# Performance work log

Measured on AMD Instinct MI355X. Metric: run time of the kernel, lower is better.

## Reference

```python
import jax, jax.numpy as jnp
import numpy as np

N_EMBD = 768
N_HEAD = 12
HEAD_DIM = N_EMBD // N_HEAD


def setup_inputs() -> dict:
    key = jax.random.key(0)
    k0, k1, k2, k3, k4 = jax.random.split(key, 5)
    B, T, C = 2, 4096, N_EMBD
    x = jax.random.normal(k0, (B, T, C), dtype=jnp.float32)
    # c_attn: Linear(C, 3C); c_proj: Linear(C, C). torch Linear: y = x @ W.T + b
    s = 1.0 / np.sqrt(C)
    W_attn = jax.random.uniform(k1, (3 * C, C), dtype=jnp.float32, minval=-s, maxval=s)
    b_attn = jax.random.uniform(k2, (3 * C,), dtype=jnp.float32, minval=-s, maxval=s)
    W_proj = jax.random.uniform(k3, (C, C), dtype=jnp.float32, minval=-s, maxval=s)
    b_proj = jax.random.uniform(k4, (C,), dtype=jnp.float32, minval=-s, maxval=s)
    return {"x": x, "W_attn": W_attn, "b_attn": b_attn, "W_proj": W_proj, "b_proj": b_proj}


def reference(x, W_attn, b_attn, W_proj, b_proj):
    B, T, C = x.shape
    H, D = N_HEAD, HEAD_DIM
    qkv = x @ W_attn.T + b_attn                      # [B,T,3C]
    q, k, v = jnp.split(qkv, 3, axis=-1)
    # [B,T,C] -> [B,H,T,D]
    q = q.reshape(B, T, H, D).transpose(0, 2, 1, 3)
    k = k.reshape(B, T, H, D).transpose(0, 2, 1, 3)
    v = v.reshape(B, T, H, D).transpose(0, 2, 1, 3)
    scale = 1.0 / jnp.sqrt(jnp.asarray(D, dtype=x.dtype))
    att = jnp.einsum('bhqd,bhkd->bhqk', q, k) * scale  # [B,H,T,T]
    att = jax.nn.softmax(att, axis=-1)
    y = jnp.einsum('bhqk,bhkd->bhqd', att, v)          # [B,H,T,D]
    y = y.transpose(0, 2, 1, 3).reshape(B, T, C)
    return y @ W_proj.T + b_proj
```

## Files before the change

kernel.cpp:

```cpp
#include <hip/hip_runtime.h>
#include <stdint.h>
#include <stddef.h>

typedef __bf16 bf16_t;
typedef bf16_t bf16x4 __attribute__((ext_vector_type(4)));
typedef bf16_t bf16x8 __attribute__((ext_vector_type(8)));
typedef float  f32x4  __attribute__((ext_vector_type(4)));
typedef _Float16 f16_t;
typedef f16_t f16x2 __attribute__((ext_vector_type(2)));
typedef f16_t f16x4 __attribute__((ext_vector_type(4)));
typedef __fp16 fp16x2_raw __attribute__((ext_vector_type(2)));

__device__ __forceinline__ f16x2 pkrtz(float a, float b) {
    fp16x2_raw r = __builtin_amdgcn_cvt_pkrtz(a, b);
    union { fp16x2_raw r; f16x2 h; } u;
    u.r = r;
    return u.h;
}

#define MFMA_BF16_K32(a, b, c) __builtin_amdgcn_mfma_f32_16x16x32_bf16(a, b, c, 0, 0, 0)
#define MFMA_F16_K16(a, b, c)  __builtin_amdgcn_mfma_f32_16x16x16f16(a, b, c, 0, 0, 0)

__device__ __forceinline__ void gload_lds16(const void* g, void* l) {
    __builtin_amdgcn_global_load_lds(
        (const __attribute__((address_space(1))) void*)g,
        (__attribute__((address_space(3))) void*)l,
        16, 0, 0);
}

#define NX 1572864
#define NWA 442368
#define NWP 147456
__global__ void cvt_all(const float* __restrict__ x, const float* __restrict__ Wa,
                        const float* __restrict__ Wp, bf16_t* __restrict__ xb,
                        bf16_t* __restrict__ Wab, bf16_t* __restrict__ Wpb) {
    int i = blockIdx.x * blockDim.x + threadIdx.x;
    const float4* src; bf16_t* dst; int j;
    if (i < NX)            { src = (const float4*)x;  dst = xb;  j = i; }
    else if (i < NX + NWA) { src = (const float4*)Wa; dst = Wab; j = i - NX; }
    else                   { src = (const float4*)Wp; dst = Wpb; j = i - NX - NWA; }
    float4 f = src[j];
    bf16x4 o = { (bf16_t)f.x, (bf16_t)f.y, (bf16_t)f.z, (bf16_t)f.w };
    ((bf16x4*)dst)[j] = o;
}

template <int KDIM>
__device__ __forceinline__ void gemm_mainloop(
    const bf16_t* __restrict__ A, const bf16_t* __restrict__ Bt,
    bf16_t* As, bf16_t* Bs, int m0, int n0, int wave, int lane, f32x4 acc[4][4])
{
    const int quad = lane >> 4, l15 = lane & 15;
    const int wm = ((wave >> 1) << 6), wn = ((wave & 1) << 6);

    const int srow = (wave << 4) + (lane >> 2);
    const int sw   = (((lane & 3) ^ ((srow >> 1) & 3)) << 3);
    const bf16_t* gA = A  + (size_t)(m0 + srow) * KDIM + sw;
    const bf16_t* gB = Bt + (size_t)(n0 + srow) * KDIM + sw;
    bf16_t* lA0 = As + wave * 512;
    bf16_t* lA1 = As + 2048 + wave * 512;
    bf16_t* lB0 = Bs + wave * 512;
    bf16_t* lB1 = Bs + 2048 + wave * 512;

    const int xorv = ((quad ^ ((l15 >> 1) & 3)) << 3);

    for (int k0 = 0; k0 < KDIM; k0 += 32) {
        __syncthreads();
        gload_lds16(gA + k0,                       lA0);
        gload_lds16(gA + (size_t)64 * KDIM + k0,   lA1);
        gload_lds16(gB + k0,                       lB0);
        gload_lds16(gB + (size_t)64 * KDIM + k0,   lB1);
        __syncthreads();

        bf16x8 af[4], bfr[4];
#pragma unroll
        for (int t = 0; t < 4; t++) {
            af[t]  = *(const bf16x8*)(As + (wm + t * 16 + l15) * 32 + xorv);
            bfr[t] = *(const bf16x8*)(Bs + (wn + t * 16 + l15) * 32 + xorv);
        }
#pragma unroll
        for (int mt = 0; mt < 4; mt++)
#pragma unroll
            for (int nt = 0; nt < 4; nt++)
                acc[mt][nt] = MFMA_BF16_K32(af[mt], bfr[nt], acc[mt][nt]);
    }
}

__global__ __launch_bounds__(256) void gemm_qkv(
    const bf16_t* __restrict__ A,
    const bf16_t* __restrict__ Bt,
    const float* __restrict__ bias,
    bf16_t* __restrict__ qo, bf16_t* __restrict__ ko, f16_t* __restrict__ vo)
{
    __shared__ bf16_t As[128 * 32];
    __shared__ bf16_t Bs[128 * 32];
    const int tid = threadIdx.x, wave = tid >> 6, lane = tid & 63;
    const int quad = lane >> 4, l15 = lane & 15;
    const int m0 = blockIdx.y * 128, n0 = blockIdx.x * 128;
    f32x4 acc[4][4] = {};
    gemm_mainloop<768>(A, Bt, As, Bs, m0, n0, wave, lane, acc);

    const int wm = ((wave >> 1) << 6), wn = ((wave & 1) << 6);
#pragma unroll
    for (int nt = 0; nt < 4; nt++) {
        const int cc = n0 + wn + nt * 16 + l15;
        const float bia = bias[cc];
        const int which = cc / 768;
        const int rem = cc - which * 768;
        const int h = rem >> 6, d = rem & 63;
        if (which < 2) {
            bf16_t* dst = (which == 0) ? qo : ko;
#pragma unroll
            for (int mt = 0; mt < 4; mt++) {
#pragma unroll
                for (int r = 0; r < 4; r++) {
                    const int row = m0 + wm + mt * 16 + quad * 4 + r;
                    const int b = row >> 12, t = row & 4095;
                    dst[((size_t)(b * 12 + h) * 4096 + t) * 64 + d] =
                        (bf16_t)(acc[mt][nt][r] + bia);
                }
            }
        } else {
#pragma unroll
            for (int mt = 0; mt < 4; mt++) {
                const int row0 = m0 + wm + mt * 16 + quad * 4;
                const int b = row0 >> 12, t0 = row0 & 4095;
                f16x4 ov = { (f16_t)(acc[mt][nt][0] + bia),
                             (f16_t)(acc[mt][nt][1] + bia),
                             (f16_t)(acc[mt][nt][2] + bia),
                             (f16_t)(acc[mt][nt][3] + bia) };
                *(f16x4*)(vo + ((size_t)(b * 12 + h) * 64 + d) * 4096 + t0) = ov;
            }
        }
    }
}

__global__ __launch_bounds__(256) void gemm_proj(
    const bf16_t* __restrict__ A,
    const bf16_t* __restrict__ Bt,
    const float* __restrict__ bias,
    float* __restrict__ out)
{
    __shared__ bf16_t As[128 * 32];
    __shared__ bf16_t Bs[128 * 32];
    const int tid = threadIdx.x, wave = tid >> 6, lane = tid & 63;
    const int quad = lane >> 4, l15 = lane & 15;
    const int m0 = blockIdx.y * 128, n0 = blockIdx.x * 128;
    f32x4 acc[4][4] = {};
    gemm_mainloop<768>(A, Bt, As, Bs, m0, n0, wave, lane, acc);

    const int wm = ((wave >> 1) << 6), wn = ((wave & 1) << 6);
#pragma unroll
    for (int nt = 0; nt < 4; nt++) {
        const int cc = n0 + wn + nt * 16 + l15;
        const float bia = bias[cc];
#pragma unroll
        for (int mt = 0; mt < 4; mt++) {
#pragma unroll
            for (int r = 0; r < 4; r++) {
                const int row = m0 + wm + mt * 16 + quad * 4 + r;
                out[(size_t)row * 768 + cc] = acc[mt][nt][r] + bia;
            }
        }
    }
}

#define QSCALE 0.1803368801f
__global__ __launch_bounds__(256, 3) void attn_fwd(
    const bf16_t* __restrict__ qg, const bf16_t* __restrict__ kg,
    const f16_t* __restrict__ vtg, bf16_t* __restrict__ y)
{
    __shared__ __align__(16) char smem[36608];
    bf16_t* Ks0 = (bf16_t*)(smem);
    bf16_t* Ks1 = (bf16_t*)(smem + 8192);
    f16_t*  Vt0 = (f16_t*)(smem + 16384);
    f16_t*  Vt1 = (f16_t*)(smem + 24576);
    float*  RedA = (float*)(smem);
    float*  RedB = (float*)(smem + 17408);
    float*  Psr  = (float*)(smem + 34816);
    float*  PsT  = (float*)(smem + 35840);

    const int tid = threadIdx.x, wave = tid >> 6, lane = tid & 63;
    const int quad = lane >> 4, l15 = lane & 15;

    const int blk = blockIdx.x;
    const int xcd = blk & 7;
    const int idx = blk >> 3;
    const int hl  = idx % 3;
    const int qt  = idx / 3;
    const int bh  = xcd * 3 + hl;
    const int b = bh / 12, h = bh - b * 12;
    const size_t base = (size_t)bh * 4096 * 64;

    bf16x8 qf[4][2];
#pragma unroll
    for (int qc = 0; qc < 4; qc++) {
        const int qrow = qt * 64 + qc * 16 + l15;
        qf[qc][0] = *(const bf16x8*)(qg + base + (size_t)qrow * 64 + quad * 8);
        qf[qc][1] = *(const bf16x8*)(qg + base + (size_t)qrow * 64 + 32 + quad * 8);
#pragma unroll
        for (int j = 0; j < 8; j++) {
            qf[qc][0][j] = (bf16_t)((float)qf[qc][0][j] * QSCALE);
            qf[qc][1][j] = (bf16_t)((float)qf[qc][1][j] * QSCALE);
        }
    }

    f32x4 O[4][4] = {};
    float psum[4] = {};
    const f16x2 one2 = { (f16_t)1.0f, (f16_t)1.0f };

    const int srow8 = tid >> 3;
    const int sc8   = (tid & 7) ^ (srow8 & 7);
    const int l8 = l15 & 7;
    const int w16 = wave << 4;
    const int ksoff = (quad ^ l8) << 3;
    const int vslot = ((wave << 1) | (quad >> 1)) ^ l8;
    const int q0off = (quad & 1) * 8;

    auto stage = [&](const bf16_t* kp, const f16_t* vp, bf16_t* Kd, f16_t* Vd) {
#pragma unroll
        for (int i = 0; i < 2; i++) {
            gload_lds16(kp + (i * 32 + srow8) * 64 + sc8 * 8,           Kd + (i * 256 + tid) * 8);
            gload_lds16(vp + (size_t)(i * 32 + srow8) * 4096 + sc8 * 8, Vd + (i * 256 + tid) * 8);
        }
    };

    auto compute = [&](const bf16_t* ks, const f16_t* vs) {
        const bf16_t* kr = ks + (w16 + l15) * 64;
        bf16x8 kf0 = *(const bf16x8*)(kr + ksoff);
        bf16x8 kf1 = *(const bf16x8*)(kr + (ksoff ^ 32));
        f32x4 sc[4];
#pragma unroll
        for (int qc = 0; qc < 4; qc++) {
            f32x4 s = {};
            s = MFMA_BF16_K32(kf0, qf[qc][0], s);
            s = MFMA_BF16_K32(kf1, qf[qc][1], s);
            sc[qc] = s;
        }
        f16x4 pf[4];
#pragma unroll
        for (int qc = 0; qc < 4; qc++) {
            float e0 = __builtin_amdgcn_exp2f(sc[qc][0]);
            float e1 = __builtin_amdgcn_exp2f(sc[qc][1]);
            float e2 = __builtin_amdgcn_exp2f(sc[qc][2]);
            float e3 = __builtin_amdgcn_exp2f(sc[qc][3]);
            f16x2 lo = pkrtz(e0, e1);
            f16x2 hi = pkrtz(e2, e3);
            psum[qc] = __builtin_amdgcn_fdot2(lo, one2, psum[qc], false);
            psum[qc] = __builtin_amdgcn_fdot2(hi, one2, psum[qc], false);
            f16x4 p;
            *(f16x2*)&p = lo;
            *(((f16x2*)&p) + 1) = hi;
            pf[qc] = p;
        }
#pragma unroll
        for (int dt = 0; dt < 4; dt++) {
            const char* vr = (const char*)(vs + (dt * 16 + l15) * 64);
            f16x4 vf = *(const f16x4*)(vr + vslot * 16 + q0off);
#pragma unroll
            for (int qc = 0; qc < 4; qc++)
                O[dt][qc] = MFMA_F16_K16(vf, pf[qc], O[dt][qc]);
        }
    };

    const bf16_t* kp = kg + base;
    const f16_t*  vp = vtg + base;
    stage(kp, vp, Ks0, Vt0); kp += 4096; vp += 64;
    for (int kt = 0; kt < 64; kt += 2) {
        __syncthreads();
        stage(kp, vp, Ks1, Vt1); kp += 4096; vp += 64;
        compute(Ks0, Vt0);
        __syncthreads();
        if (kt + 2 < 64) { stage(kp, vp, Ks0, Vt0); kp += 4096; vp += 64; }
        compute(Ks1, Vt1);
    }

#pragma unroll
    for (int qc = 0; qc < 4; qc++) {
        psum[qc] += __shfl_xor(psum[qc], 16, 64);
        psum[qc] += __shfl_xor(psum[qc], 32, 64);
    }
    __syncthreads();
    if (wave == 2) {
#pragma unroll
        for (int dt = 0; dt < 4; dt++)
#pragma unroll
            for (int qc = 0; qc < 4; qc++)
                *(f32x4*)(RedA + (qc * 16 + l15) * 68 + dt * 16 + quad * 4) = O[dt][qc];
    } else if (wave == 3) {
#pragma unroll
        for (int dt = 0; dt < 4; dt++)
#pragma unroll
            for (int qc = 0; qc < 4; qc++)
                *(f32x4*)(RedB + (qc * 16 + l15) * 68 + dt * 16 + quad * 4) = O[dt][qc];
    }
    if (quad == 0) {
#pragma unroll
        for (int qc = 0; qc < 4; qc++) Psr[wave * 64 + qc * 16 + l15] = psum[qc];
    }
    __syncthreads();
    if (wave == 0) {
#pragma unroll
        for (int dt = 0; dt < 4; dt++)
#pragma unroll
            for (int qc = 0; qc < 4; qc++)
                O[dt][qc] += *(const f32x4*)(RedA + (qc * 16 + l15) * 68 + dt * 16 + quad * 4);
    } else if (wave == 1) {
#pragma unroll
        for (int dt = 0; dt < 4; dt++)
#pragma unroll
            for (int qc = 0; qc < 4; qc++)
                O[dt][qc] += *(const f32x4*)(RedB + (qc * 16 + l15) * 68 + dt * 16 + quad * 4);
    }
    __syncthreads();
    if (wave == 1) {
#pragma unroll
        for (int dt = 0; dt < 4; dt++)
#pragma unroll
            for (int qc = 0; qc < 4; qc++)
                *(f32x4*)(RedA + (qc * 16 + l15) * 68 + dt * 16 + quad * 4) = O[dt][qc];
    } else if (wave == 3) {
        PsT[lane] = Psr[lane] + Psr[64 + lane] + Psr[128 + lane] + Psr[192 + lane];
    }
    __syncthreads();
    if (wave == 0) {
#pragma unroll
        for (int qc = 0; qc < 4; qc++) {
            const float rcp = 1.0f / PsT[qc * 16 + l15];
            const int t = qt * 64 + qc * 16 + l15;
            bf16_t* yr = y + ((size_t)b * 4096 + t) * 768 + h * 64 + quad * 4;
#pragma unroll
            for (int dt = 0; dt < 4; dt++) {
                f32x4 o4 = O[dt][qc] +
                    *(const f32x4*)(RedA + (qc * 16 + l15) * 68 + dt * 16 + quad * 4);
                bf16x4 ov = { (bf16_t)(o4[0] * rcp), (bf16_t)(o4[1] * rcp),
                              (bf16_t)(o4[2] * rcp), (bf16_t)(o4[3] * rcp) };
                *(bf16x4*)(yr + dt * 16) = ov;
            }
        }
    }
}

extern "C" void kernel_launch(void* const* d_in, const int* in_sizes, int n_in,
                              void* d_out, int out_size, void* d_ws, size_t ws_size,
                              hipStream_t stream) {
    const float* x  = (const float*)d_in[0];
    const float* Wa = (const float*)d_in[1];
    const float* ba = (const float*)d_in[2];
    const float* Wp = (const float*)d_in[3];
    const float* bp = (const float*)d_in[4];
    float* out = (float*)d_out;

    char* ws = (char*)d_ws;
    bf16_t* xb  = (bf16_t*)(ws);
    bf16_t* Wab = (bf16_t*)(ws + 12582912);
    bf16_t* Wpb = (bf16_t*)(ws + 16121856);
    bf16_t* qb  = (bf16_t*)(ws + 17301504);
    bf16_t* kb  = (bf16_t*)(ws + 29884416);
    f16_t*  vtb = (f16_t*)(ws + 42467328);
    bf16_t* yb  = (bf16_t*)(ws + 55050240);

    cvt_all<<<8448, 256, 0, stream>>>(x, Wa, Wp, xb, Wab, Wpb);
    gemm_qkv <<<dim3(18, 64), 256, 0, stream>>>(xb, Wab, ba, qb, kb, vtb);
    attn_fwd <<<1536, 256, 0, stream>>>(qb, kb, vtb, yb);
    gemm_proj<<<dim3( 6, 64), 256, 0, stream>>>(yb, Wpb, bp, out);
}
```

Measured before the change: 275.6 us.

## Process key tiles in pairs using 16x16x32 f16 MFMA with deeper staging

The attention kernel now handles two 64-key tiles per compute step. Their P fragments and V fragments are concatenated so the PV product uses the K=32 f16 MFMA instead of two K=16 MFMAs. Shared memory grows to 64KB for four K/V buffers, and s_setprio raises wave priority around the MFMA sections. The larger LDS footprint and the launch bound dropping from 3 to 2 blocks per CU lower occupancy, which could hurt latency hiding.

```diff
diff --git a/kernel.cpp b/kernel.cpp
--- a/kernel.cpp
+++ b/kernel.cpp
@@ -9,6 +9,7 @@
 typedef _Float16 f16_t;
 typedef f16_t f16x2 __attribute__((ext_vector_type(2)));
 typedef f16_t f16x4 __attribute__((ext_vector_type(4)));
+typedef f16_t f16x8 __attribute__((ext_vector_type(8)));
 typedef __fp16 fp16x2_raw __attribute__((ext_vector_type(2)));
 
 __device__ __forceinline__ f16x2 pkrtz(float a, float b) {
@@ -19,7 +20,7 @@
 }
 
 #define MFMA_BF16_K32(a, b, c) __builtin_amdgcn_mfma_f32_16x16x32_bf16(a, b, c, 0, 0, 0)
-#define MFMA_F16_K16(a, b, c)  __builtin_amdgcn_mfma_f32_16x16x16f16(a, b, c, 0, 0, 0)
+#define MFMA_F16_K32(a, b, c)  __builtin_amdgcn_mfma_f32_16x16x32_f16(a, b, c, 0, 0, 0)
 
 __device__ __forceinline__ void gload_lds16(const void* g, void* l) {
     __builtin_amdgcn_global_load_lds(
@@ -165,15 +166,19 @@
 }
 
 #define QSCALE 0.1803368801f
-__global__ __launch_bounds__(256, 3) void attn_fwd(
+__global__ __launch_bounds__(256, 2) void attn_fwd(
     const bf16_t* __restrict__ qg, const bf16_t* __restrict__ kg,
     const f16_t* __restrict__ vtg, bf16_t* __restrict__ y)
 {
-    __shared__ __align__(16) char smem[36608];
+    __shared__ __align__(16) char smem[65536];
     bf16_t* Ks0 = (bf16_t*)(smem);
     bf16_t* Ks1 = (bf16_t*)(smem + 8192);
-    f16_t*  Vt0 = (f16_t*)(smem + 16384);
-    f16_t*  Vt1 = (f16_t*)(smem + 24576);
+    bf16_t* Ks2 = (bf16_t*)(smem + 16384);
+    bf16_t* Ks3 = (bf16_t*)(smem + 24576);
+    f16_t*  Vt0 = (f16_t*)(smem + 32768);
+    f16_t*  Vt1 = (f16_t*)(smem + 40960);
+    f16_t*  Vt2 = (f16_t*)(smem + 49152);
+    f16_t*  Vt3 = (f16_t*)(smem + 57344);
     float*  RedA = (float*)(smem);
     float*  RedB = (float*)(smem + 17408);
     float*  Psr  = (float*)(smem + 34816);
@@ -216,62 +221,96 @@
     const int vslot = ((wave << 1) | (quad >> 1)) ^ l8;
     const int q0off = (quad & 1) * 8;
 
-    auto stage = [&](const bf16_t* kp, const f16_t* vp, bf16_t* Kd, f16_t* Vd) {
+    auto stage = [&](const bf16_t* kp_, const f16_t* vp_, bf16_t* Kd, f16_t* Vd) {
 #pragma unroll
         for (int i = 0; i < 2; i++) {
-            gload_lds16(kp + (i * 32 + srow8) * 64 + sc8 * 8,           Kd + (i * 256 + tid) * 8);
-            gload_lds16(vp + (size_t)(i * 32 + srow8) * 4096 + sc8 * 8, Vd + (i * 256 + tid) * 8);
+            gload_lds16(kp_ + (i * 32 + srow8) * 64 + sc8 * 8,           Kd + (i * 256 + tid) * 8);
+            gload_lds16(vp_ + (size_t)(i * 32 + srow8) * 4096 + sc8 * 8, Vd + (i * 256 + tid) * 8);
         }
     };
 
-    auto compute = [&](const bf16_t* ks, const f16_t* vs) {
-        const bf16_t* kr = ks + (w16 + l15) * 64;
-        bf16x8 kf0 = *(const bf16x8*)(kr + ksoff);
-        bf16x8 kf1 = *(const bf16x8*)(kr + (ksoff ^ 32));
-        f32x4 sc[4];
+    auto compute_pair = [&](const bf16_t* ksA, const f16_t* vsA,
+                            const bf16_t* ksB, const f16_t* vsB) {
+        const bf16_t* krA = ksA + (w16 + l15) * 64;
+        const bf16_t* krB = ksB + (w16 + l15) * 64;
+        bf16x8 kfA0 = *(const bf16x8*)(krA + ksoff);
+        bf16x8 kfA1 = *(const bf16x8*)(krA + (ksoff ^ 32));
+        bf16x8 kfB0 = *(const bf16x8*)(krB + ksoff);
+        bf16x8 kfB1 = *(const bf16x8*)(krB + (ksoff ^ 32));
+        f32x4 scA[4], scB[4];
+        __builtin_amdgcn_s_setprio(1);
 #pragma unroll
         for (int qc = 0; qc < 4; qc++) {
             f32x4 s = {};
-            s = MFMA_BF16_K32(kf0, qf[qc][0], s);
-            s = MFMA_BF16_K32(kf1, qf[qc][1], s);
-            sc[qc] = s;
-        }
-        f16x4 pf[4];
+            s = MFMA_BF16_K32(kfA0, qf[qc][0], s);
+            s = MFMA_BF16_K32(kfA1, qf[qc][1], s);
+            scA[qc] = s;
+        }
 #pragma unroll
         for (int qc = 0; qc < 4; qc++) {
-            float e0 = __builtin_amdgcn_exp2f(sc[qc][0]);
-            float e1 = __builtin_amdgcn_exp2f(sc[qc][1]);
-            float e2 = __builtin_amdgcn_exp2f(sc[qc][2]);
-            float e3 = __builtin_amdgcn_exp2f(sc[qc][3]);
-            f16x2 lo = pkrtz(e0, e1);
-            f16x2 hi = pkrtz(e2, e3);
-            psum[qc] = __builtin_amdgcn_fdot2(lo, one2, psum[qc], false);
-            psum[qc] = __builtin_amdgcn_fdot2(hi, one2, psum[qc], false);
-            f16x4 p;
-            *(f16x2*)&p = lo;
-            *(((f16x2*)&p) + 1) = hi;
-            pf[qc] = p;
-        }
+            f32x4 s = {};
+            s = MFMA_BF16_K32(kfB0, qf[qc][0], s);
+            s = MFMA_BF16_K32(kfB1, qf[qc][1], s);
+            scB[qc] = s;
+        }
+        __builtin_amdgcn_s_setprio(0);
+        f16x8 pf8[4];
+#pragma unroll
+        for (int qc = 0; qc < 4; qc++) {
+            float a0 = __builtin_amdgcn_exp2f(scA[qc][0]);
+            float a1 = __builtin_amdgcn_exp2f(scA[qc][1]);
+            float a2 = __builtin_amdgcn_exp2f(scA[qc][2]);
+            float a3 = __builtin_amdgcn_exp2f(scA[qc][3]);
+            float b0 = __builtin_amdgcn_exp2f(scB[qc][0]);
+            float b1 = __builtin_amdgcn_exp2f(scB[qc][1]);
+            float b2 = __builtin_amdgcn_exp2f(scB[qc][2]);
+            float b3 = __builtin_amdgcn_exp2f(scB[qc][3]);
+            f16x2 loA = pkrtz(a0, a1);
+            f16x2 hiA = pkrtz(a2, a3);
+            f16x2 loB = pkrtz(b0, b1);
+            f16x2 hiB = pkrtz(b2, b3);
+            psum[qc] = __builtin_amdgcn_fdot2(loA, one2, psum[qc], false);
+            psum[qc] = __builtin_amdgcn_fdot2(hiA, one2, psum[qc], false);
+            psum[qc] = __builtin_amdgcn_fdot2(loB, one2, psum[qc], false);
+            psum[qc] = __builtin_amdgcn_fdot2(hiB, one2, psum[qc], false);
+            union { f16x8 v; f16x2 h[4]; } u;
+            u.h[0] = loA; u.h[1] = hiA; u.h[2] = loB; u.h[3] = hiB;
+            pf8[qc] = u.v;
+        }
+        __builtin_amdgcn_s_setprio(1);
 #pragma unroll
         for (int dt = 0; dt < 4; dt++) {
-            const char* vr = (const char*)(vs + (dt * 16 + l15) * 64);
-            f16x4 vf = *(const f16x4*)(vr + vslot * 16 + q0off);
-#pragma unroll
-            for (int qc = 0; qc < 4; qc++)
-                O[dt][qc] = MFMA_F16_K16(vf, pf[qc], O[dt][qc]);
-        }
+            const char* vrA = (const char*)(vsA + (dt * 16 + l15) * 64);
+            const char* vrB = (const char*)(vsB + (dt * 16 + l15) * 64);
+            f16x4 vA = *(const f16x4*)(vrA + vslot * 16 + q0off);
+            f16x4 vB = *(const f16x4*)(vrB + vslot * 16 + q0off);
+            union { f16x8 v; f16x4 h[2]; } uv;
+            uv.h[0] = vA; uv.h[1] = vB;
+#pragma unroll
+            for (int qc = 0; qc < 4; qc++)
+                O[dt][qc] = MFMA_F16_K32(uv.v, pf8[qc], O[dt][qc]);
+        }
+        __builtin_amdgcn_s_setprio(0);
     };
 
     const bf16_t* kp = kg + base;
     const f16_t*  vp = vtg + base;
-    stage(kp, vp, Ks0, Vt0); kp += 4096; vp += 64;
-    for (int kt = 0; kt < 64; kt += 2) {
+    stage(kp, vp, Ks0, Vt0);
+    stage(kp + 4096, vp + 64, Ks1, Vt1);
+    kp += 8192; vp += 128;
+    for (int pt = 0; pt < 32; pt += 2) {
         __syncthreads();
-        stage(kp, vp, Ks1, Vt1); kp += 4096; vp += 64;
-        compute(Ks0, Vt0);
+        stage(kp, vp, Ks2, Vt2);
+        stage(kp + 4096, vp + 64, Ks3, Vt3);
+        kp += 8192; vp += 128;
+        compute_pair(Ks0, Vt0, Ks1, Vt1);
         __syncthreads();
-        if (kt + 2 < 64) { stage(kp, vp, Ks0, Vt0); kp += 4096; vp += 64; }
-        compute(Ks1, Vt1);
+        if (pt + 2 < 32) {
+            stage(kp, vp, Ks0, Vt0);
+            stage(kp + 4096, vp + 64, Ks1, Vt1);
+            kp += 8192; vp += 128;
+        }
+        compute_pair(Ks2, Vt2, Ks3, Vt3);
     }
 
 #pragma unroll
```

Result: no change. 273.6 us (-0.7%).
